# Optimization experiments

Hardware: AMD Instinct MI355X
Metric: run time of the kernel (lower is better)

Reference implementation:

```python
import jax, jax.numpy as jnp
import numpy as np

H = 16  # num_heads


def setup_inputs() -> dict:
    key = jax.random.key(0)
    ks = jax.random.split(key, 8)
    B, S, d, L = 1, 2048, 1024, 8
    hd = d // H
    s = 0.02
    return {
        "x": jax.random.normal(ks[0], (B, S, d), jnp.float32),
        "past_values": jax.random.normal(ks[1], (L, B, H, S, hd), jnp.float32),
        "Wqkv": jax.random.normal(ks[2], (3 * d, d), jnp.float32) * s,
        "bqkv": jax.random.normal(ks[3], (3 * d,), jnp.float32) * s,
        "Wcol": jax.random.normal(ks[4], (d, d), jnp.float32) * s,
        "bcol": jax.random.normal(ks[5], (d,), jnp.float32) * s,
        "Wout": jax.random.normal(ks[6], (d, d), jnp.float32) * s,
        "bout": jax.random.normal(ks[7], (d,), jnp.float32) * s,
    }


def reference(x, past_values, Wqkv, bqkv, Wcol, bcol, Wout, bout):
    B, S, d = x.shape
    L = past_values.shape[0]
    hd = d // H
    scale = 1.0 / np.sqrt(hd).astype(np.float32)

    qkv = x @ Wqkv.T + bqkv                       # [B,S,3d]
    q, k, v = jnp.split(qkv, 3, axis=-1)

    def heads(t):                                  # [B,S,d] -> [B,H,S,hd]
        return t.reshape(B, S, H, hd).transpose(0, 2, 1, 3)

    q_row, k, v = heads(q), heads(k), heads(v)
    q_col = heads(x @ Wcol.T + bcol)

    # causal token scores [B,H,S,S]
    token_scores = jnp.einsum('bhqd,bhkd->bhqk', q_row, k) * scale
    causal = jnp.triu(jnp.ones((S, S), bool), 1)
    token_scores = jnp.where(causal, -jnp.inf, token_scores)

    # stack past values: torch stack(dim=3) -> [B,H,S,L,hd]; permute -> [B,S,L,H*hd]
    pv = past_values.transpose(1, 3, 0, 2, 4).reshape(B, S, L, d)
    ri = pv.reshape(B, S * L, d)
    mu = ri.mean(-1, keepdims=True)
    var = ri.var(-1, keepdims=True)
    ri = (ri - mu) / jnp.sqrt(var + 1e-5)          # F.layer_norm, no affine

    Wk, bk = Wqkv[d:2 * d], bqkv[d:2 * d]
    Wv, bv = Wqkv[2 * d:], bqkv[2 * d:]
    rk = (ri @ Wk.T + bk).reshape(B, S * L, H, hd).transpose(0, 2, 1, 3).reshape(B, H, S, L, hd)
    rv = (ri @ Wv.T + bv).reshape(B, S * L, H, hd).transpose(0, 2, 1, 3).reshape(B, H, S, L, hd)

    mem_scores = jnp.einsum('bhsd,bhsld->bhsl', q_col, rk) * scale  # [B,H,S,L]

    scores = jnp.concatenate([token_scores, mem_scores], axis=-1)   # [B,H,S,S+L]
    w = jax.nn.softmax(scores, axis=-1)
    tw, mw = w[..., :S], w[..., S:]

    ctx = jnp.einsum('bhqk,bhkd->bhqd', tw, v) + jnp.einsum('bhsl,bhsld->bhsd', mw, rv)
    out = ctx.transpose(0, 2, 1, 3).reshape(B, S, d)
    return out @ Wout.T + bout
```

## Files before the change

kernel.cpp:

```cpp
#include <hip/hip_runtime.h>
#include <math.h>

#define D   1024
#define H   16
#define HD  64
#define SEQ 2048
#define LL  8
#define SCALE 0.125f

typedef __attribute__((ext_vector_type(8))) __bf16 bf16x8;
typedef __attribute__((ext_vector_type(4))) float floatx4;
typedef __attribute__((ext_vector_type(8))) unsigned short ushort8;

__device__ inline unsigned short f32_to_bf16(float f) {
    unsigned int u = __builtin_bit_cast(unsigned int, f);
    u += 0x7FFF + ((u >> 16) & 1);
    return (unsigned short)(u >> 16);
}
__device__ inline float bf2f(unsigned short u) {
    unsigned int x = (unsigned int)u << 16;
    return __builtin_bit_cast(float, x);
}
__device__ inline void load_lds16(const void* g, void* l) {
    __builtin_amdgcn_global_load_lds(
        (__attribute__((address_space(1))) void*)g,
        (__attribute__((address_space(3))) void*)l, 16, 0, 0);
}

__device__ inline void xcd_swizzle(int& bx, int& by) {
    const int gx   = gridDim.x;
    const int lin  = blockIdx.y * gx + blockIdx.x;
    const int nblk = gx * gridDim.y;
    const int virt = (lin & 7) * (nblk >> 3) + (lin >> 3);
    bx = virt % gx;
    by = virt / gx;
}

#define NQ_X    524288
#define NQ_WQKV 786432
#define NQ_WC   262144
#define NQ_WO   262144
#define LN_BLK  16384
#define CVT_BLK 7168
#define PREP_GRID (LN_BLK + CVT_BLK + 4)

__global__ __launch_bounds__(256) void prep_kernel(
    const float* __restrict__ pv, const float* __restrict__ x,
    const float* __restrict__ Wqkv, const float* __restrict__ Wcol,
    const float* __restrict__ Wout, const float* __restrict__ bqkv,
    const float* __restrict__ bcol,
    unsigned short* __restrict__ ri, unsigned short* __restrict__ xb,
    unsigned short* __restrict__ W4b, unsigned short* __restrict__ Woutb,
    float* __restrict__ b4)
{
    const int b = blockIdx.x;
    const int t = threadIdx.x;
    if (b < LN_BLK) {
        const int r = b;
        const int s = r >> 3, l = r & 7;
        const int h = t >> 4, e = (t & 15) * 4;
        const size_t src = (size_t)l * (H * SEQ * HD) + (size_t)h * (SEQ * HD)
                         + (size_t)s * HD + e;
        float4 v = *(const float4*)(pv + src);
        float sum = v.x + v.y + v.z + v.w;
        float sq  = v.x * v.x + v.y * v.y + v.z * v.z + v.w * v.w;
#pragma unroll
        for (int off = 32; off; off >>= 1) {
            sum += __shfl_xor(sum, off);
            sq  += __shfl_xor(sq, off);
        }
        __shared__ float red[8];
        if ((t & 63) == 0) { red[(t >> 6) * 2] = sum; red[(t >> 6) * 2 + 1] = sq; }
        __syncthreads();
        sum = red[0] + red[2] + red[4] + red[6];
        sq  = red[1] + red[3] + red[5] + red[7];
        const float mean = sum * (1.f / 1024.f);
        const float var  = sq * (1.f / 1024.f) - mean * mean;
        const float rstd = rsqrtf(var + 1e-5f);
        ushort4 o;
        o.x = f32_to_bf16((v.x - mean) * rstd);
        o.y = f32_to_bf16((v.y - mean) * rstd);
        o.z = f32_to_bf16((v.z - mean) * rstd);
        o.w = f32_to_bf16((v.w - mean) * rstd);
        *(ushort4*)(ri + (size_t)r * D + t * 4) = o;
    } else if (b < LN_BLK + CVT_BLK) {
        const int i = (b - LN_BLK) * 256 + t;
        const float* src; unsigned short* dst; int off;
        if (i < NQ_X)                        { src = x;    dst = xb;    off = i; }
        else if (i < NQ_X + NQ_WQKV)         { src = Wqkv; dst = W4b;   off = i - NQ_X; }
        else if (i < NQ_X + NQ_WQKV + NQ_WC) {
            float4 v = ((const float4*)Wcol)[i - NQ_X - NQ_WQKV];
            ushort4 o;
            o.x = f32_to_bf16(v.x); o.y = f32_to_bf16(v.y);
            o.z = f32_to_bf16(v.z); o.w = f32_to_bf16(v.w);
            ((ushort4*)(W4b))[NQ_WQKV + (i - NQ_X - NQ_WQKV)] = o;
            return;
        }
        else                                 { src = Wout; dst = Woutb; off = i - NQ_X - NQ_WQKV - NQ_WC; }
        float4 v = ((const float4*)src)[off];
        ushort4 o;
        o.x = f32_to_bf16(v.x); o.y = f32_to_bf16(v.y);
        o.z = f32_to_bf16(v.z); o.w = f32_to_bf16(v.w);
        ((ushort4*)dst)[off] = o;
    } else {
        const int q = (b - LN_BLK - CVT_BLK) * 256 + t;
        float4 v = (q < 768) ? ((const float4*)bqkv)[q] : ((const float4*)bcol)[q - 768];
        ((float4*)b4)[q] = v;
    }
}

__global__ __launch_bounds__(256) void wkt_kernel(
    const float* __restrict__ Wqkv, unsigned short* __restrict__ WkT)
{
    const int h = blockIdx.x >> 4, ct = blockIdx.x & 15;
    const int c0 = ct * 64;
    const int t = threadIdx.x;
    __shared__ float tile[64][68];
    {
        const int e  = t >> 2;
        const int c4 = (t & 3) * 16;
        const float* src = Wqkv + (size_t)(D + h * HD + e) * D + c0 + c4;
#pragma unroll
        for (int j = 0; j < 4; j++) {
            float4 v = ((const float4*)src)[j];
            *(float4*)&tile[e][c4 + j * 4] = v;
        }
    }
    __syncthreads();
    {
        const int c  = t >> 2;
        const int e0 = (t & 3) * 16;
        ushort8 o0, o1;
#pragma unroll
        for (int j = 0; j < 8; j++) o0[j] = f32_to_bf16(tile[e0 + j][c]);
#pragma unroll
        for (int j = 0; j < 8; j++) o1[j] = f32_to_bf16(tile[e0 + 8 + j][c]);
        unsigned short* dst = WkT + (size_t)h * (D * HD) + (size_t)(c0 + c) * HD + e0;
        *(ushort8*)dst       = o0;
        *(ushort8*)(dst + 8) = o1;
    }
}

__global__ __launch_bounds__(256) void vtr_kernel(
    const unsigned short* __restrict__ qkv4, unsigned short* __restrict__ VT)
{
    const int h = blockIdx.x & 15, kt = blockIdx.x >> 4;
    const int t = threadIdx.x;
    __shared__ unsigned short Vt[64][264];
    const int pr = t & 31, eg = t >> 5;
#pragma unroll
    for (int sub = 0; sub < 4; sub++) {
        const int j0 = kt * 256 + sub * 64;
        const unsigned short* v0 = qkv4 + (size_t)(j0 + 2 * pr) * 4096 + 2 * D + h * HD + eg * 8;
        ushort8 va = *(const ushort8*)v0;
        ushort8 vb = *(const ushort8*)(v0 + 4096);
#pragma unroll
        for (int j = 0; j < 8; j++) {
            unsigned int pk = (unsigned int)va[j] | ((unsigned int)vb[j] << 16);
            *(unsigned int*)&Vt[eg * 8 + j][sub * 64 + 2 * pr] = pk;
        }
    }
    __syncthreads();
#pragma unroll
    for (int it = 0; it < 8; it++) {
        const int idx = it * 256 + t;
        const int e = idx >> 5, ch = idx & 31;
        ushort8 v = *(const ushort8*)&Vt[e][ch * 8];
        *(ushort8*)(VT + (size_t)h * (HD * SEQ) + (size_t)e * SEQ + kt * 256 + ch * 8) = v;
    }
}

template <typename CT, bool HAS_BIAS>
__global__ __launch_bounds__(256) void gemm_bf16_kernel(
    const unsigned short* __restrict__ A, const unsigned short* __restrict__ W,
    const float* __restrict__ bias, CT* __restrict__ C,
    int K, int N, int lda, int ldw, int ldc,
    size_t zsA, size_t zsW, size_t zsC)
{
    A += (size_t)blockIdx.z * zsA;
    W += (size_t)blockIdx.z * zsW;
    C += (size_t)blockIdx.z * zsC;

    __shared__ unsigned short As[128 * 32];
    __shared__ unsigned short Ws[128 * 32];
    const int t    = threadIdx.x;
    const int wave = t >> 6, lane = t & 63;
    const int wm   = wave >> 1, wn = wave & 1;
    int bx, by;
    xcd_swizzle(bx, by);
    const int m0 = by * 128, n0 = bx * 128;

    floatx4 acc[4][4];
#pragma unroll
    for (int i = 0; i < 4; i++)
#pragma unroll
        for (int j = 0; j < 4; j++) acc[i][j] = (floatx4)0.f;

    const int lrow = lane >> 2;
    const int lcol = (lane & 3) * 8;
    const unsigned short* Ag = A + (size_t)(m0 + wave * 32 + lrow) * lda + lcol;
    const unsigned short* Wg = W + (size_t)(n0 + wave * 32 + lrow) * ldw + lcol;
    unsigned short* Asw = &As[wave * 32 * 32];
    unsigned short* Wsw = &Ws[wave * 32 * 32];
    const size_t rowskipA = (size_t)16 * lda;
    const size_t rowskipW = (size_t)16 * ldw;

    const int arow  = lane & 15;
    const int aquad = (lane >> 4) * 8;

    for (int k0 = 0; k0 < K; k0 += 32) {
        load_lds16(Ag + k0,             Asw);
        load_lds16(Ag + k0 + rowskipA,  Asw + 16 * 32);
        load_lds16(Wg + k0,             Wsw);
        load_lds16(Wg + k0 + rowskipW,  Wsw + 16 * 32);
        __syncthreads();

        bf16x8 af[4], wf[4];
#pragma unroll
        for (int mi = 0; mi < 4; mi++)
            af[mi] = *(const bf16x8*)&As[(wm * 64 + mi * 16 + arow) * 32 + aquad];
#pragma unroll
        for (int ni = 0; ni < 4; ni++)
            wf[ni] = *(const bf16x8*)&Ws[(wn * 64 + ni * 16 + arow) * 32 + aquad];
#pragma unroll
        for (int mi = 0; mi < 4; mi++)
#pragma unroll
            for (int ni = 0; ni < 4; ni++)
                acc[mi][ni] = __builtin_amdgcn_mfma_f32_16x16x32_bf16(
                    af[mi], wf[ni], acc[mi][ni], 0, 0, 0);
        __syncthreads();
    }

    const int crow = (lane >> 4) * 4, ccol = lane & 15;
#pragma unroll
    for (int mi = 0; mi < 4; mi++) {
#pragma unroll
        for (int ni = 0; ni < 4; ni++) {
            const int gm = m0 + wm * 64 + mi * 16 + crow;
            const int gn = n0 + wn * 64 + ni * 16 + ccol;
            float bb = 0.f;
            if constexpr (HAS_BIAS) bb = bias[gn];
#pragma unroll
            for (int r = 0; r < 4; r++) {
                float v = acc[mi][ni][r] + bb;
                if constexpr (sizeof(CT) == 2)
                    C[(size_t)(gm + r) * ldc + gn] = (CT)f32_to_bf16(v);
                else
                    C[(size_t)(gm + r) * ldc + gn] = v;
            }
        }
    }
}

#define RI_STRIDE 1032

__global__ __launch_bounds__(256) void memsc_kernel(
    const unsigned short* __restrict__ U, const unsigned short* __restrict__ ri,
    const unsigned short* __restrict__ qkv4, const float* __restrict__ bqkv,
    float* __restrict__ scores)
{
    const int s = blockIdx.x;
    const int t = threadIdx.x;
    __shared__ unsigned short riS[LL * RI_STRIDE];
    __shared__ float qbS[H];
    {
        const unsigned short* src = ri + (size_t)s * (LL * D);
#pragma unroll
        for (int j = 0; j < 4; j++) {
            const int off = (j * 256 + t) * 8;
            const int l = off >> 10, c = off & 1023;
            ushort8 v = *(const ushort8*)(src + off);
            *(ushort8*)&riS[l * RI_STRIDE + c] = v;
        }
    }
    {
        const int h = t >> 4, sub = t & 15;
        const unsigned short* qc = qkv4 + (size_t)s * 4096 + 3 * D + h * HD + sub * 4;
        const float* bk = bqkv + D + h * HD + sub * 4;
        float acc = 0.f;
#pragma unroll
        for (int j = 0; j < 4; j++) acc += bf2f(qc[j]) * bk[j];
#pragma unroll
        for (int off = 1; off < 16; off <<= 1) acc += __shfl_xor(acc, off);
        if (sub == 0) qbS[h] = acc;
    }
    __syncthreads();
    const int p = t >> 1, half = t & 1;
    const int h = p >> 3, l = p & 7;
    const unsigned short* Up = U + ((size_t)h * SEQ + s) * D + half * 512;
    const unsigned short* rp = &riS[l * RI_STRIDE + half * 512];
    float acc = 0.f;
#pragma unroll 4
    for (int j = 0; j < 64; j++) {
        ushort8 u = *(const ushort8*)(Up + j * 8);
        ushort8 r = *(const ushort8*)(rp + j * 8);
#pragma unroll
        for (int k = 0; k < 8; k++) acc += bf2f(u[k]) * bf2f(r[k]);
    }
    acc += __shfl_xor(acc, 1);
    if (half == 0)
        scores[((size_t)s * H + h) * LL + l] = (acc + qbS[h]) * SCALE;
}

__global__ __launch_bounds__(256, 3) void attn_split_kernel(
    const unsigned short* __restrict__ qkv4, const unsigned short* __restrict__ VT,
    float* __restrict__ Opart, float2* __restrict__ mlpart)
{
    const int t    = threadIdx.x;
    const int w    = t >> 6, lane = t & 63;
    const int lrow = lane & 15;
    const int lk   = (lane >> 4) * 8;
    const int rrow = (lane >> 4) * 4;
    const int lin  = blockIdx.x;
    const int hsp  = lin & 63, g = lin >> 6;
    const int s    = hsp >> 4, h = hsp & 15;
    const int qt   = 31 - g;
    const int q0   = qt * 64;
    const int n    = qt + 1;
    const int lo   = (s * n) >> 2, hi = ((s + 1) * n) >> 2;
    const int part = (h * 32 + qt) * 4 + s;

    __shared__ unsigned short Ks[2][64 * 72];
    __shared__ unsigned short Vs[2][64 * 72];
    __shared__ unsigned short Pb[4][16 * 72];
    unsigned short* Pw = Pb[w];

    bf16x8 qreg[2];
#pragma unroll
    for (int kst = 0; kst < 2; kst++) {
        ushort8 qu = *(const ushort8*)(qkv4 + (size_t)(q0 + w * 16 + lrow) * 4096
                                       + h * HD + kst * 32 + lk);
        ushort8 qs;
#pragma unroll
        for (int j = 0; j < 8; j++) qs[j] = f32_to_bf16(bf2f(qu[j]) * SCALE);
        qreg[kst] = __builtin_bit_cast(bf16x8, qs);
    }

    const int srow = t >> 3;
    const int scol = (t & 7) * 8;
    const unsigned short* Kg = qkv4 + D + h * HD;
    const unsigned short* Vg = VT + (size_t)h * (HD * SEQ);

    bf16x8 kr0, kr1, vr0, vr1;
    float m_i[4], l_i[4];
    floatx4 Oacc[4];
#pragma unroll
    for (int r = 0; r < 4; r++) { m_i[r] = -1e30f; l_i[r] = 0.f; }
#pragma unroll
    for (int et = 0; et < 4; et++) Oacc[et] = (floatx4)0.f;

    if (lo < hi) {
        const int j0 = lo * 64;
        kr0 = *(const bf16x8*)(Kg + (size_t)(j0 + srow) * 4096 + scol);
        kr1 = *(const bf16x8*)(Kg + (size_t)(j0 + 32 + srow) * 4096 + scol);
        vr0 = *(const bf16x8*)(Vg + (size_t)srow * SEQ + j0 + scol);
        vr1 = *(const bf16x8*)(Vg + (size_t)(srow + 32) * SEQ + j0 + scol);
    }

    int cur = 0;
    for (int jt = lo; jt < hi; jt++) {
        const int j0 = jt * 64;
        *(bf16x8*)&Ks[cur][srow * 72 + scol]        = kr0;
        *(bf16x8*)&Ks[cur][(srow + 32) * 72 + scol] = kr1;
        *(bf16x8*)&Vs[cur][srow * 72 + scol]        = vr0;
        *(bf16x8*)&Vs[cur][(srow + 32) * 72 + scol] = vr1;
        if (jt + 1 < hi) {
            const int j0n = (jt + 1) * 64;
            kr0 = *(const bf16x8*)(Kg + (size_t)(j0n + srow) * 4096 + scol);
            kr1 = *(const bf16x8*)(Kg + (size_t)(j0n + 32 + srow) * 4096 + scol);
            vr0 = *(const bf16x8*)(Vg + (size_t)srow * SEQ + j0n + scol);
            vr1 = *(const bf16x8*)(Vg + (size_t)(srow + 32) * SEQ + j0n + scol);
        }
        __syncthreads();

        floatx4 S[4];
#pragma unroll
        for (int nt = 0; nt < 4; nt++) S[nt] = (floatx4)0.f;
        __builtin_amdgcn_s_setprio(1);
#pragma unroll
        for (int kst = 0; kst < 2; kst++) {
#pragma unroll
            for (int nt = 0; nt < 4; nt++) {
                bf16x8 bk = *(const bf16x8*)&Ks[cur][(nt * 16 + lrow) * 72 + kst * 32 + lk];
                S[nt] = __builtin_amdgcn_mfma_f32_16x16x32_bf16(qreg[kst], bk, S[nt], 0, 0, 0);
            }
        }
        __builtin_amdgcn_s_setprio(0);

        if (jt != qt) {
#pragma unroll
            for (int r = 0; r < 4; r++) {
                float sc[4];
#pragma unroll
                for (int nt = 0; nt < 4; nt++) sc[nt] = S[nt][r];
                float mx = fmaxf(fmaxf(sc[0], sc[1]), fmaxf(sc[2], sc[3]));
#pragma unroll
                for (int off = 1; off < 16; off <<= 1)
                    mx = fmaxf(mx, __shfl_xor(mx, off));
                const bool keep = __all(mx <= m_i[r] + 8.f);
                const float newm = keep ? m_i[r] : fmaxf(m_i[r], mx);
                float ps = 0.f;
#pragma unroll
                for (int nt = 0; nt < 4; nt++) {
                    float pe = __expf(sc[nt] - newm);
                    ps += pe;
                    Pw[(rrow + r) * 72 + nt * 16 + lrow] = f32_to_bf16(pe);
                }
#pragma unroll
                for (int off = 1; off < 16; off <<= 1)
                    ps += __shfl_xor(ps, off);
                if (keep) {
                    l_i[r] += ps;
                } else {
                    const float alpha = __expf(m_i[r] - newm);
                    m_i[r] = newm;
                    l_i[r] = l_i[r] * alpha + ps;
#pragma unroll
                    for (int et = 0; et < 4; et++) Oacc[et][r] *= alpha;
                }
            }
        } else {
#pragma unroll
            for (int r = 0; r < 4; r++) {
                const int qg = q0 + w * 16 + rrow + r;
                float sc[4];
                float mx = -1e30f;
#pragma unroll
                for (int nt = 0; nt < 4; nt++) {
                    sc[nt] = S[nt][r];
                    if (j0 + nt * 16 + lrow > qg) sc[nt] = -1e30f;
                    mx = fmaxf(mx, sc[nt]);
                }
#pragma unroll
                for (int off = 1; off < 16; off <<= 1)
                    mx = fmaxf(mx, __shfl_xor(mx, off));
                const float newm  = fmaxf(m_i[r], mx);
                const float alpha = __expf(m_i[r] - newm);
                m_i[r] = newm;
                float ps = 0.f;
#pragma unroll
                for (int nt = 0; nt < 4; nt++) {
                    float pe = __expf(sc[nt] - newm);
                    ps += pe;
                    Pw[(rrow + r) * 72 + nt * 16 + lrow] = f32_to_bf16(pe);
                }
#pragma unroll
                for (int off = 1; off < 16; off <<= 1)
                    ps += __shfl_xor(ps, off);
                l_i[r] = l_i[r] * alpha + ps;
#pragma unroll
                for (int et = 0; et < 4; et++) Oacc[et][r] *= alpha;
            }
        }

        __builtin_amdgcn_s_setprio(1);
#pragma unroll
        for (int kst = 0; kst < 2; kst++) {
            bf16x8 ap = *(const bf16x8*)&Pw[lrow * 72 + kst * 32 + lk];
#pragma unroll
            for (int et = 0; et < 4; et++) {
                bf16x8 bv = *(const bf16x8*)&Vs[cur][(et * 16 + lrow) * 72 + kst * 32 + lk];
                Oacc[et] = __builtin_amdgcn_mfma_f32_16x16x32_bf16(ap, bv, Oacc[et], 0, 0, 0);
            }
        }
        __builtin_amdgcn_s_setprio(0);
        cur ^= 1;
    }

#pragma unroll
    for (int r = 0; r < 4; r++) {
        const int ql = w * 16 + rrow + r;
        if (lrow == 0) mlpart[(size_t)part * 64 + ql] = make_float2(m_i[r], l_i[r]);
#pragma unroll
        for (int et = 0; et < 4; et++)
            Opart[((size_t)part * 64 + ql) * 64 + et * 16 + lrow] = Oacc[et][r];
    }
}

__global__ __launch_bounds__(256) void attn_merge_kernel(
    const float* __restrict__ Opart, const float2* __restrict__ mlpart,
    const float* __restrict__ scores,
    float* __restrict__ tok, float* __restrict__ mwf, float* __restrict__ Pmem)
{
    const int blk = blockIdx.x;
    const int h = blk >> 5, qt = blk & 31;
    const int q0 = qt * 64;
    const int t = threadIdx.x, tx = t & 15, ty = t >> 4;
    const size_t pb = (size_t)blk * 4;
#pragma unroll
    for (int i = 0; i < 4; i++) {
        const int qi = ty * 4 + i, qg = q0 + qi;
        float2 ml[4];
#pragma unroll
        for (int ps = 0; ps < 4; ps++) ml[ps] = mlpart[(pb + ps) * 64 + qi];
        const float* msp = scores + ((size_t)qg * H + h) * LL;
        float ms[LL];
#pragma unroll
        for (int l = 0; l < LL; l++) ms[l] = msp[l];
        float M = ml[0].x;
#pragma unroll
        for (int ps = 1; ps < 4; ps++) M = fmaxf(M, ml[ps].x);
#pragma unroll
        for (int l = 0; l < LL; l++) M = fmaxf(M, ms[l]);
        float f[4], L = 0.f;
#pragma unroll
        for (int ps = 0; ps < 4; ps++) { f[ps] = __expf(ml[ps].x - M); L += ml[ps].y * f[ps]; }
        float pm[LL];
#pragma unroll
        for (int l = 0; l < LL; l++) { pm[l] = __expf(ms[l] - M); L += pm[l]; }
        const float rl = 1.f / L;
        float4 o = make_float4(0.f, 0.f, 0.f, 0.f);
#pragma unroll
        for (int ps = 0; ps < 4; ps++) {
            const float fs = f[ps] * rl;
            float4 op = *(const float4*)&Opart[((pb + ps) * 64 + qi) * 64 + tx * 4];
            o.x += op.x * fs; o.y += op.y * fs; o.z += op.z * fs; o.w += op.w * fs;
        }
        *(float4*)&tok[(size_t)qg * D + h * HD + tx * 4] = o;
        if (tx == 0) {
            float* mw = mwf + ((size_t)qg * H + h) * LL;
            float psum = 0.f;
#pragma unroll
            for (int l = 0; l < LL; l++) { float v = pm[l] * rl; mw[l] = v; psum += v; }
            Pmem[(size_t)qg * H + h] = psum;
        }
    }
}

__global__ __launch_bounds__(256) void rbar_kernel(
    const float* __restrict__ mwf, const unsigned short* __restrict__ ri,
    unsigned short* __restrict__ rbar)
{
    const int s = blockIdx.x, t = threadIdx.x;
    __shared__ unsigned short riS[LL * D];
    __shared__ float wS[H * LL];
    {
        const unsigned short* src = ri + (size_t)s * (LL * D);
#pragma unroll
        for (int j = 0; j < 4; j++) {
            const int off = (j * 256 + t) * 8;
            *(ushort8*)&riS[off] = *(const ushort8*)(src + off);
        }
    }
    if (t < H * LL) wS[t] = mwf[(size_t)s * (H * LL) + t];
    __syncthreads();
    const int c4 = t * 4;
#pragma unroll
    for (int hh = 0; hh < H; hh++) {
        float v0 = 0.f, v1 = 0.f, v2 = 0.f, v3 = 0.f;
#pragma unroll
        for (int l = 0; l < LL; l++) {
            const float wv = wS[hh * LL + l];
            ushort4 rr = *(const ushort4*)&riS[l * D + c4];
            v0 += wv * bf2f(rr.x); v1 += wv * bf2f(rr.y);
            v2 += wv * bf2f(rr.z); v3 += wv * bf2f(rr.w);
        }
        ushort4 o;
        o.x = f32_to_bf16(v0); o.y = f32_to_bf16(v1);
        o.z = f32_to_bf16(v2); o.w = f32_to_bf16(v3);
        *(ushort4*)(rbar + ((size_t)hh * SEQ + s) * D + c4) = o;
    }
}

__global__ __launch_bounds__(256) void gemm_ctx_kernel(
    const unsigned short* __restrict__ rbar, const unsigned short* __restrict__ W4,
    const float* __restrict__ bqkv, const float* __restrict__ Pmem,
    const float* __restrict__ tok, unsigned short* __restrict__ ctx)
{
    const int mt = blockIdx.x;
    const int h  = blockIdx.y;
    const unsigned short* A  = rbar + (size_t)h * SEQ * D + (size_t)mt * 128 * D;
    const unsigned short* Wv = W4 + (size_t)(2 * D + h * HD) * D;
    const float* bv = bqkv + 2 * D + h * HD;

    __shared__ unsigned short As[128 * 32];
    __shared__ unsigned short Ws[64 * 32];
    const int t    = threadIdx.x;
    const int wave = t >> 6, lane = t & 63;

    floatx4 acc[2][4];
#pragma unroll
    for (int i = 0; i < 2; i++)
#pragma unroll
        for (int j = 0; j < 4; j++) acc[i][j] = (floatx4)0.f;

    const int lrow = lane >> 2;
    const int lcol = (lane & 3) * 8;
    const unsigned short* Ag = A  + (size_t)(wave * 32 + lrow) * D + lcol;
    const unsigned short* Wg = Wv + (size_t)(wave * 32 + lrow) * D + lcol;
    unsigned short* Asw = &As[wave * 32 * 32];
    unsigned short* Wsw = &Ws[wave * 32 * 32];
    const size_t rowskip = (size_t)16 * D;

    const int arow  = lane & 15;
    const int aquad = (lane >> 4) * 8;

    for (int k0 = 0; k0 < D; k0 += 32) {
        load_lds16(Ag + k0,           Asw);
        load_lds16(Ag + k0 + rowskip, Asw + 16 * 32);
        if (wave < 2) {
            load_lds16(Wg + k0,           Wsw);
            load_lds16(Wg + k0 + rowskip, Wsw + 16 * 32);
        }
        __syncthreads();

        bf16x8 af[2], wf[4];
#pragma unroll
        for (int mi = 0; mi < 2; mi++)
            af[mi] = *(const bf16x8*)&As[(wave * 32 + mi * 16 + arow) * 32 + aquad];
#pragma unroll
        for (int ni = 0; ni < 4; ni++)
            wf[ni] = *(const bf16x8*)&Ws[(ni * 16 + arow) * 32 + aquad];
#pragma unroll
        for (int mi = 0; mi < 2; mi++)
#pragma unroll
            for (int ni = 0; ni < 4; ni++)
                acc[mi][ni] = __builtin_amdgcn_mfma_f32_16x16x32_bf16(
                    af[mi], wf[ni], acc[mi][ni], 0, 0, 0);
        __syncthreads();
    }

    const int crow = (lane >> 4) * 4, ccol = lane & 15;
#pragma unroll
    for (int mi = 0; mi < 2; mi++) {
#pragma unroll
        for (int ni = 0; ni < 4; ni++) {
            const int e  = ni * 16 + ccol;
            const float bb = bv[e];
#pragma unroll
            for (int r = 0; r < 4; r++) {
                const int grow = mt * 128 + wave * 32 + mi * 16 + crow + r;
                float v = acc[mi][ni][r] + bb * Pmem[(size_t)grow * H + h]
                          + tok[(size_t)grow * D + h * HD + e];
                ctx[(size_t)grow * D + h * HD + e] = f32_to_bf16(v);
            }
        }
    }
}

extern "C" void kernel_launch(void* const* d_in, const int* in_sizes, int n_in,
                              void* d_out, int out_size, void* d_ws, size_t ws_size,
                              hipStream_t stream)
{
    const float* x    = (const float*)d_in[0];
    const float* pv   = (const float*)d_in[1];
    const float* Wqkv = (const float*)d_in[2];
    const float* bqkv = (const float*)d_in[3];
    const float* Wcol = (const float*)d_in[4];
    const float* bcol = (const float*)d_in[5];
    const float* Wout = (const float*)d_in[6];
    const float* bout = (const float*)d_in[7];
    float* out = (float*)d_out;

    char* p = (char*)d_ws;
    unsigned short* x_bf    = (unsigned short*)p; p += (size_t)2048 * 1024 * 2;
    unsigned short* W4_bf   = (unsigned short*)p; p += (size_t)4096 * 1024 * 2;
    unsigned short* Wout_bf = (unsigned short*)p; p += (size_t)1024 * 1024 * 2;
    float*          b4      = (float*)p;          p += (size_t)4096 * 4;
    unsigned short* ri_bf   = (unsigned short*)p; p += (size_t)16384 * 1024 * 2;
    unsigned short* qkv4_bf = (unsigned short*)p; p += (size_t)2048 * 4096 * 2;
    unsigned short* WkT_bf  = (unsigned short*)p; p += (size_t)16 * 1024 * 64 * 2;
    unsigned short* VT_bf   = (unsigned short*)p; p += (size_t)16 * 64 * 2048 * 2;
    float*          scores  = (float*)p;          p += (size_t)2048 * 16 * 8 * 4;
    float*          mwf     = (float*)p;          p += (size_t)2048 * 16 * 8 * 4;
    float*          Pmem    = (float*)p;          p += (size_t)2048 * 16 * 4;
    float*          tok     = (float*)p;          p += (size_t)2048 * 1024 * 4;
    unsigned short* ctx_bf  = (unsigned short*)p; p += (size_t)2048 * 1024 * 2;
    float*          Opart   = (float*)p;          p += (size_t)2048 * 64 * 64 * 4;
    float2*         mlpart  = (float2*)p;         p += (size_t)2048 * 64 * 8;
    unsigned short* Urb     = (unsigned short*)p; p += (size_t)16 * 2048 * 1024 * 2;

    prep_kernel<<<PREP_GRID, 256, 0, stream>>>(pv, x, Wqkv, Wcol, Wout, bqkv, bcol,
                                               ri_bf, x_bf, W4_bf, Wout_bf, b4);
    wkt_kernel<<<256, 256, 0, stream>>>(Wqkv, WkT_bf);
    gemm_bf16_kernel<unsigned short, true><<<dim3(32, 16, 1), 256, 0, stream>>>(
        x_bf, W4_bf, b4, qkv4_bf, 1024, 4096, 1024, 1024, 4096, 0, 0, 0);
    vtr_kernel<<<128, 256, 0, stream>>>(qkv4_bf, VT_bf);
    gemm_bf16_kernel<unsigned short, false><<<dim3(8, 16, 16), 256, 0, stream>>>(
        qkv4_bf + 3 * D, WkT_bf, nullptr, Urb, 64, 1024, 4096, 64, 1024,
        (size_t)HD, (size_t)D * HD, (size_t)SEQ * D);
    memsc_kernel<<<2048, 256, 0, stream>>>(Urb, ri_bf, qkv4_bf, bqkv, scores);
    attn_split_kernel<<<2048, 256, 0, stream>>>(qkv4_bf, VT_bf, Opart, mlpart);
    attn_merge_kernel<<<512, 256, 0, stream>>>(Opart, mlpart, scores, tok, mwf, Pmem);
    rbar_kernel<<<2048, 256, 0, stream>>>(mwf, ri_bf, Urb);
    gemm_ctx_kernel<<<dim3(16, 16), 256, 0, stream>>>(Urb, W4_bf, bqkv, Pmem, tok, ctx_bf);
    gemm_bf16_kernel<float, true><<<dim3(8, 16, 1), 256, 0, stream>>>(
        ctx_bf, Wout_bf, bout, out, 1024, 1024, 1024, 1024, 1024, 0, 0, 0);
}
```

Measured before the change: 338.4 us.

## Store U per token and compute memory scores with MFMA from LDS

```diff
diff --git a/kernel.cpp b/kernel.cpp
--- a/kernel.cpp
+++ b/kernel.cpp
@@ -252,7 +252,7 @@
     }
 }
 
-#define RI_STRIDE 1032
+#define US_STRIDE 1032
 
 __global__ __launch_bounds__(256) void memsc_kernel(
     const unsigned short* __restrict__ U, const unsigned short* __restrict__ ri,
@@ -261,16 +261,35 @@
 {
     const int s = blockIdx.x;
     const int t = threadIdx.x;
-    __shared__ unsigned short riS[LL * RI_STRIDE];
+    const int w = t >> 6, lane = t & 63;
+    const int lrow = lane & 15;
+    const int lkq  = (lane >> 4) * 8;
+
+    __shared__ unsigned short Us[16 * US_STRIDE];
+    __shared__ union {
+        unsigned short riS[8 * US_STRIDE];
+        float red[4][16][16];
+    } R;
     __shared__ float qbS[H];
+
+    {
+        const unsigned short* src = U + (size_t)s * (H * D);
+#pragma unroll
+        for (int j = 0; j < 8; j++) {
+            const int c = j * 256 + t;
+            const int row = c >> 7, col = (c & 127) * 8;
+            *(ushort8*)&Us[row * US_STRIDE + col] =
+                *(const ushort8*)(src + row * D + col);
+        }
+    }
     {
         const unsigned short* src = ri + (size_t)s * (LL * D);
 #pragma unroll
         for (int j = 0; j < 4; j++) {
-            const int off = (j * 256 + t) * 8;
-            const int l = off >> 10, c = off & 1023;
-            ushort8 v = *(const ushort8*)(src + off);
-            *(ushort8*)&riS[l * RI_STRIDE + c] = v;
+            const int c = j * 256 + t;
+            const int row = c >> 7, col = (c & 127) * 8;
+            *(ushort8*)&R.riS[row * US_STRIDE + col] =
+                *(const ushort8*)(src + row * D + col);
         }
     }
     {
@@ -285,21 +304,31 @@
         if (sub == 0) qbS[h] = acc;
     }
     __syncthreads();
-    const int p = t >> 1, half = t & 1;
-    const int h = p >> 3, l = p & 7;
-    const unsigned short* Up = U + ((size_t)h * SEQ + s) * D + half * 512;
-    const unsigned short* rp = &riS[l * RI_STRIDE + half * 512];
-    float acc = 0.f;
-#pragma unroll 4
-    for (int j = 0; j < 64; j++) {
-        ushort8 u = *(const ushort8*)(Up + j * 8);
-        ushort8 r = *(const ushort8*)(rp + j * 8);
-#pragma unroll
-        for (int k = 0; k < 8; k++) acc += bf2f(u[k]) * bf2f(r[k]);
-    }
-    acc += __shfl_xor(acc, 1);
-    if (half == 0)
-        scores[((size_t)s * H + h) * LL + l] = (acc + qbS[h]) * SCALE;
+
+    floatx4 acc = (floatx4)0.f;
+    const int kbase = w * 256;
+#pragma unroll
+    for (int step = 0; step < 8; step++) {
+        const int k0 = kbase + step * 32;
+        bf16x8 af = *(const bf16x8*)&Us[lrow * US_STRIDE + k0 + lkq];
+        bf16x8 bf = {};
+        if (lrow < 8) bf = *(const bf16x8*)&R.riS[lrow * US_STRIDE + k0 + lkq];
+        acc = __builtin_amdgcn_mfma_f32_16x16x32_bf16(af, bf, acc, 0, 0, 0);
+    }
+    __syncthreads();
+
+    {
+        const int crow = (lane >> 4) * 4, ccol = lane & 15;
+#pragma unroll
+        for (int r = 0; r < 4; r++) R.red[w][crow + r][ccol] = acc[r];
+    }
+    __syncthreads();
+
+    if (t < H * LL) {
+        const int h = t >> 3, l = t & 7;
+        float v = R.red[0][h][l] + R.red[1][h][l] + R.red[2][h][l] + R.red[3][h][l];
+        scores[((size_t)s * H + h) * LL + l] = (v + qbS[h]) * SCALE;
+    }
 }
 
 __global__ __launch_bounds__(256, 3) void attn_split_kernel(
@@ -677,8 +706,8 @@
         x_bf, W4_bf, b4, qkv4_bf, 1024, 4096, 1024, 1024, 4096, 0, 0, 0);
     vtr_kernel<<<128, 256, 0, stream>>>(qkv4_bf, VT_bf);
     gemm_bf16_kernel<unsigned short, false><<<dim3(8, 16, 16), 256, 0, stream>>>(
-        qkv4_bf + 3 * D, WkT_bf, nullptr, Urb, 64, 1024, 4096, 64, 1024,
-        (size_t)HD, (size_t)D * HD, (size_t)SEQ * D);
+        qkv4_bf + 3 * D, WkT_bf, nullptr, Urb, 64, 1024, 4096, 64, H * D,
+        (size_t)HD, (size_t)D * HD, (size_t)D);
     memsc_kernel<<<2048, 256, 0, stream>>>(Urb, ri_bf, qkv4_bf, bqkv, scores);
     attn_split_kernel<<<2048, 256, 0, stream>>>(qkv4_bf, VT_bf, Opart, mlpart);
     attn_merge_kernel<<<512, 256, 0, stream>>>(Opart, mlpart, scores, tok, mwf, Pmem);
```

New measurement: 319.4 us. 1.06x faster.
